# Kernel optimization log

Measured on AMD Instinct MI355X. Metric: run time of the kernel, lower is better.

Reference implementation:

```python
import jax, jax.numpy as jnp
import numpy as np

IN_CH = 256
OUT_CH = 128
N = 6144
ADJ_P = 0.01  # edge density -> avg degree ~61


def setup_inputs() -> dict:
    key = jax.random.key(0)
    ks = jax.random.split(key, 8)
    x = jax.random.normal(ks[0], (1, IN_CH, N), dtype=jnp.float32)
    adj = (jax.random.uniform(ks[1], (N, N)) < ADJ_P).astype(jnp.float32)
    W_fts = jax.random.normal(ks[2], (OUT_CH, IN_CH), dtype=jnp.float32) * 0.05
    w1 = jax.random.normal(ks[3], (OUT_CH,), dtype=jnp.float32) * 0.05
    b1 = jnp.zeros((1,), dtype=jnp.float32)
    w2 = jax.random.normal(ks[4], (OUT_CH,), dtype=jnp.float32) * 0.05
    b2 = jnp.zeros((1,), dtype=jnp.float32)
    vars_bias = jax.random.normal(ks[5], (1, N, OUT_CH), dtype=jnp.float32) * 0.02
    return {"x": x, "adj": adj, "W_fts": W_fts, "w1": w1, "b1": b1,
            "w2": w2, "b2": b2, "vars_bias": vars_bias}


def reference(x, adj, W_fts, w1, b1, w2, b2, vars_bias):
    # fts = Conv1d(in, out, k=1, bias=False)(x): [1, OUT_CH, N]
    fts = jnp.einsum('oi,bin->bon', W_fts, x)
    f = fts[0]  # [OUT_CH, N]
    # f1/f2 = Conv1d(out, 1, 1)(fts) -> per-node scalars [N]
    f1 = jnp.einsum('o,on->n', w1, f) + b1  # [N]
    f2 = jnp.einsum('o,on->n', w2, f) + b2  # [N]
    # scores[i,j] = leaky_relu(adj[i,j]*f1[i] + adj[i,j]*f2[j], 0.2)
    scores = jax.nn.leaky_relu(adj * f1[:, None] + adj * f2[None, :], 0.2)
    # sparse_softmax2d: per-row softmax masked to nonzero entries
    mask = (scores != 0).astype(scores.dtype)
    m = jnp.max(scores, axis=1, keepdims=True)  # stabilizer; cancels in ratio
    exps = jnp.exp(scores - m) * mask
    coefs = exps / jnp.sum(exps, axis=1, keepdims=True)  # [N, N]
    # vals = coefs @ fts.T : [N, OUT_CH]
    vals = coefs @ f.T
    # add bias, permute to [1, OUT_CH, N]
    ret = jnp.transpose(vals[None, :, :] + vars_bias, (0, 2, 1))
    return ret
```

## Files before the change

### kernel.cpp

```cpp
#include <hip/hip_runtime.h>

#define NN  6144
#define ICH 256
#define OCH 128

__global__ __launch_bounds__(256) void k_uproj(const float* __restrict__ W,
        const float* __restrict__ w1, const float* __restrict__ w2,
        float* __restrict__ u1, float* __restrict__ u2) {
    int k = threadIdx.x;
    float a1 = 0.f, a2 = 0.f;
    for (int o = 0; o < OCH; ++o) {
        float wv = W[o * ICH + k];
        a1 = fmaf(w1[o], wv, a1);
        a2 = fmaf(w2[o], wv, a2);
    }
    u1[k] = a1;
    u2[k] = a2;
}

__global__ __launch_bounds__(256) void k_f12(const float* __restrict__ x,
        const float* __restrict__ u1, const float* __restrict__ u2,
        float* __restrict__ f1, float* __restrict__ f2) {
    const int nchunk = blockIdx.x % (NN / 256);
    const int ks     = blockIdx.x / (NN / 256);
    const int n  = nchunk * 256 + threadIdx.x;
    const int k0 = ks * 32;
    float a1 = 0.f, a2 = 0.f;
#pragma unroll
    for (int kk = 0; kk < 32; ++kk) {
        const int k = k0 + kk;
        const float xv = x[(size_t)k * NN + n];
        a1 = fmaf(u1[k], xv, a1);
        a2 = fmaf(u2[k], xv, a2);
    }
    atomicAdd(f1 + n, a1);
    atomicAdd(f2 + n, a2);
}

__global__ __launch_bounds__(256) void k_fts(const float* __restrict__ x,
        const float* __restrict__ W, float* __restrict__ ft) {
    __shared__ float xs[32][32];
    __shared__ float Ws[32][OCH + 4];
    const int n0  = blockIdx.x * 32;
    const int tid = threadIdx.x;
    const int oq = (tid & 31) * 4;
    const int nq = (tid >> 5) * 4;
    float acc[4][4] = {};
    for (int k0 = 0; k0 < ICH; k0 += 32) {
        __syncthreads();
        {
            const int nn = tid & 31;
            const int kb = tid >> 5;
#pragma unroll
            for (int r = 0; r < 4; ++r)
                xs[kb + r * 8][nn] = x[(size_t)(k0 + kb + r * 8) * NN + n0 + nn];
        }
        {
            const int kk = tid & 31;
            const int ob = tid >> 5;
#pragma unroll
            for (int r = 0; r < 16; ++r) {
                const int o = ob + r * 8;
                Ws[kk][o] = W[o * ICH + k0 + kk];
            }
        }
        __syncthreads();
#pragma unroll
        for (int kk = 0; kk < 32; ++kk) {
            const float4 xv = *(const float4*)&xs[kk][nq];
            const float4 wv = *(const float4*)&Ws[kk][oq];
            const float xa[4] = {xv.x, xv.y, xv.z, xv.w};
            const float wa[4] = {wv.x, wv.y, wv.z, wv.w};
#pragma unroll
            for (int a = 0; a < 4; ++a)
#pragma unroll
                for (int b = 0; b < 4; ++b)
                    acc[a][b] = fmaf(xa[a], wa[b], acc[a][b]);
        }
    }
#pragma unroll
    for (int a = 0; a < 4; ++a) {
        float4 v = make_float4(acc[a][0], acc[a][1], acc[a][2], acc[a][3]);
        *(float4*)&ft[(size_t)(n0 + nq + a) * OCH + oq] = v;
    }
}

__global__ __launch_bounds__(256) void k_attn(const float* __restrict__ adj,
        const float* __restrict__ ft, const float* __restrict__ f1,
        const float* __restrict__ f2, const float* __restrict__ b1,
        const float* __restrict__ b2, const float* __restrict__ vb,
        float* __restrict__ out) {
    const int lane = threadIdx.x & 63;
    const int wave = threadIdx.x >> 6;
    const int i = blockIdx.x * 4 + wave;
    const float s1  = f1[i] + b1[0];
    const float bb2 = b2[0];
    const float* arow = adj + (size_t)i * NN;
    float2 nm = make_float2(0.f, 0.f);
    float den = 0.f;
    for (int base = 0; base < NN; base += 256) {
        const int j0 = base + lane * 4;
        const float4 a4 = *(const float4*)(arow + j0);
        float e0 = 0.f, e1 = 0.f, e2 = 0.f, e3 = 0.f;
        const bool any = (a4.x != 0.f) || (a4.y != 0.f) ||
                         (a4.z != 0.f) || (a4.w != 0.f);
        if (any) {
            const float4 g = *(const float4*)(f2 + j0);
            if (a4.x != 0.f) { float s = s1 + g.x + bb2; s = s > 0.f ? s : 0.2f * s; e0 = __expf(s); }
            if (a4.y != 0.f) { float s = s1 + g.y + bb2; s = s > 0.f ? s : 0.2f * s; e1 = __expf(s); }
            if (a4.z != 0.f) { float s = s1 + g.z + bb2; s = s > 0.f ? s : 0.2f * s; e2 = __expf(s); }
            if (a4.w != 0.f) { float s = s1 + g.w + bb2; s = s > 0.f ? s : 0.2f * s; e3 = __expf(s); }
            den += e0 + e1 + e2 + e3;
        }
        unsigned long long m = __ballot(any);
        while (m) {
            const int le = __builtin_ctzll(m);
            m &= m - 1;
            const float v0 = __shfl(e0, le);
            const float v1 = __shfl(e1, le);
            const float v2 = __shfl(e2, le);
            const float v3 = __shfl(e3, le);
            const int jb = base + le * 4;
            if (v0 != 0.f) { const float2 g = *(const float2*)(ft + (size_t)(jb    ) * OCH + 2 * lane);
                             nm.x = fmaf(v0, g.x, nm.x); nm.y = fmaf(v0, g.y, nm.y); }
            if (v1 != 0.f) { const float2 g = *(const float2*)(ft + (size_t)(jb + 1) * OCH + 2 * lane);
                             nm.x = fmaf(v1, g.x, nm.x); nm.y = fmaf(v1, g.y, nm.y); }
            if (v2 != 0.f) { const float2 g = *(const float2*)(ft + (size_t)(jb + 2) * OCH + 2 * lane);
                             nm.x = fmaf(v2, g.x, nm.x); nm.y = fmaf(v2, g.y, nm.y); }
            if (v3 != 0.f) { const float2 g = *(const float2*)(ft + (size_t)(jb + 3) * OCH + 2 * lane);
                             nm.x = fmaf(v3, g.x, nm.x); nm.y = fmaf(v3, g.y, nm.y); }
        }
    }
#pragma unroll
    for (int off = 32; off > 0; off >>= 1) den += __shfl_xor(den, off);
    const float inv = 1.f / den;
    const int c0 = 2 * lane;
    const float2 bv = *(const float2*)(vb + (size_t)i * OCH + c0);
    out[(size_t)(c0    ) * NN + i] = fmaf(nm.x, inv, bv.x);
    out[(size_t)(c0 + 1) * NN + i] = fmaf(nm.y, inv, bv.y);
}

extern "C" void kernel_launch(void* const* d_in, const int* in_sizes, int n_in,
                              void* d_out, int out_size, void* d_ws, size_t ws_size,
                              hipStream_t stream) {
    const float* x   = (const float*)d_in[0];
    const float* adj = (const float*)d_in[1];
    const float* W   = (const float*)d_in[2];
    const float* w1  = (const float*)d_in[3];
    const float* b1  = (const float*)d_in[4];
    const float* w2  = (const float*)d_in[5];
    const float* b2  = (const float*)d_in[6];
    const float* vb  = (const float*)d_in[7];
    float* out = (float*)d_out;

    char* ws = (char*)d_ws;
    float* ft = (float*)ws;
    float* f1 = (float*)(ws + 3145728);
    float* f2 = (float*)(ws + 3145728 + 24576);
    float* u1 = (float*)(ws + 3145728 + 49152);
    float* u2 = u1 + 256;

    hipMemsetAsync(f1, 0, 2 * NN * sizeof(float), stream);
    k_uproj<<<1, 256, 0, stream>>>(W, w1, w2, u1, u2);
    k_f12<<<dim3((NN / 256) * 8), 256, 0, stream>>>(x, u1, u2, f1, f2);
    k_fts<<<dim3(NN / 32), 256, 0, stream>>>(x, W, ft);
    k_attn<<<dim3(NN / 4), 256, 0, stream>>>(adj, ft, f1, f2, b1, b2, vb, out);
}
```

Baseline: 311.4 us.

## Fuse f1/f2 projection into fts GEMM and queue edges per row in attention

Measured after the change: 272.3 us. 1.14x faster.

```diff
diff --git a/kernel.cpp b/kernel.cpp
--- a/kernel.cpp
+++ b/kernel.cpp
@@ -3,42 +3,14 @@
 #define NN  6144
 #define ICH 256
 #define OCH 128
-
-__global__ __launch_bounds__(256) void k_uproj(const float* __restrict__ W,
-        const float* __restrict__ w1, const float* __restrict__ w2,
-        float* __restrict__ u1, float* __restrict__ u2) {
-    int k = threadIdx.x;
-    float a1 = 0.f, a2 = 0.f;
-    for (int o = 0; o < OCH; ++o) {
-        float wv = W[o * ICH + k];
-        a1 = fmaf(w1[o], wv, a1);
-        a2 = fmaf(w2[o], wv, a2);
-    }
-    u1[k] = a1;
-    u2[k] = a2;
-}
-
-__global__ __launch_bounds__(256) void k_f12(const float* __restrict__ x,
-        const float* __restrict__ u1, const float* __restrict__ u2,
-        float* __restrict__ f1, float* __restrict__ f2) {
-    const int nchunk = blockIdx.x % (NN / 256);
-    const int ks     = blockIdx.x / (NN / 256);
-    const int n  = nchunk * 256 + threadIdx.x;
-    const int k0 = ks * 32;
-    float a1 = 0.f, a2 = 0.f;
-#pragma unroll
-    for (int kk = 0; kk < 32; ++kk) {
-        const int k = k0 + kk;
-        const float xv = x[(size_t)k * NN + n];
-        a1 = fmaf(u1[k], xv, a1);
-        a2 = fmaf(u2[k], xv, a2);
-    }
-    atomicAdd(f1 + n, a1);
-    atomicAdd(f2 + n, a2);
-}
+#define WPB 4
+#define NWIN 6
+#define QCAP 256
 
 __global__ __launch_bounds__(256) void k_fts(const float* __restrict__ x,
-        const float* __restrict__ W, float* __restrict__ ft) {
+        const float* __restrict__ W, const float* __restrict__ w1,
+        const float* __restrict__ w2, float* __restrict__ ft,
+        float* __restrict__ f1, float* __restrict__ f2) {
     __shared__ float xs[32][32];
     __shared__ float Ws[32][OCH + 4];
     const int n0  = blockIdx.x * 32;
@@ -83,6 +55,29 @@
         float4 v = make_float4(acc[a][0], acc[a][1], acc[a][2], acc[a][3]);
         *(float4*)&ft[(size_t)(n0 + nq + a) * OCH + oq] = v;
     }
+    const float4 w1v = *(const float4*)(w1 + oq);
+    const float4 w2v = *(const float4*)(w2 + oq);
+    float p1[4], p2[4];
+#pragma unroll
+    for (int a = 0; a < 4; ++a) {
+        p1[a] = acc[a][0] * w1v.x + acc[a][1] * w1v.y + acc[a][2] * w1v.z + acc[a][3] * w1v.w;
+        p2[a] = acc[a][0] * w2v.x + acc[a][1] * w2v.y + acc[a][2] * w2v.z + acc[a][3] * w2v.w;
+    }
+#pragma unroll
+    for (int m = 16; m > 0; m >>= 1) {
+#pragma unroll
+        for (int a = 0; a < 4; ++a) {
+            p1[a] += __shfl_xor(p1[a], m);
+            p2[a] += __shfl_xor(p2[a], m);
+        }
+    }
+    if ((tid & 31) == 0) {
+#pragma unroll
+        for (int a = 0; a < 4; ++a) {
+            f1[n0 + nq + a] = p1[a];
+            f2[n0 + nq + a] = p2[a];
+        }
+    }
 }
 
 __global__ __launch_bounds__(256) void k_attn(const float* __restrict__ adj,
@@ -90,54 +85,68 @@
         const float* __restrict__ f2, const float* __restrict__ b1,
         const float* __restrict__ b2, const float* __restrict__ vb,
         float* __restrict__ out) {
-    const int lane = threadIdx.x & 63;
-    const int wave = threadIdx.x >> 6;
-    const int i = blockIdx.x * 4 + wave;
-    const float s1  = f1[i] + b1[0];
-    const float bb2 = b2[0];
+    __shared__ float q_e[QCAP];
+    __shared__ int   q_j[QCAP];
+    __shared__ int   cnt;
+    __shared__ float dpart[WPB];
+    __shared__ float part[WPB][OCH];
+    const int tid  = threadIdx.x;
+    const int lane = tid & 63;
+    const int wave = tid >> 6;
+    const int i = blockIdx.x;
+    if (tid == 0) cnt = 0;
+    __syncthreads();
+    const float s1 = f1[i] + b1[0] + b2[0];
     const float* arow = adj + (size_t)i * NN;
-    float2 nm = make_float2(0.f, 0.f);
+    const int jbase = wave * (NN / WPB) + lane * 4;
+    float4 a[NWIN];
+#pragma unroll
+    for (int w = 0; w < NWIN; ++w)
+        a[w] = *(const float4*)(arow + jbase + w * 256);
     float den = 0.f;
-    for (int base = 0; base < NN; base += 256) {
-        const int j0 = base + lane * 4;
-        const float4 a4 = *(const float4*)(arow + j0);
-        float e0 = 0.f, e1 = 0.f, e2 = 0.f, e3 = 0.f;
-        const bool any = (a4.x != 0.f) || (a4.y != 0.f) ||
-                         (a4.z != 0.f) || (a4.w != 0.f);
-        if (any) {
+#pragma unroll
+    for (int w = 0; w < NWIN; ++w) {
+        const float4 a4 = a[w];
+        const int j0 = jbase + w * 256;
+        const int k = (a4.x != 0.f) + (a4.y != 0.f) + (a4.z != 0.f) + (a4.w != 0.f);
+        if (k) {
             const float4 g = *(const float4*)(f2 + j0);
-            if (a4.x != 0.f) { float s = s1 + g.x + bb2; s = s > 0.f ? s : 0.2f * s; e0 = __expf(s); }
-            if (a4.y != 0.f) { float s = s1 + g.y + bb2; s = s > 0.f ? s : 0.2f * s; e1 = __expf(s); }
-            if (a4.z != 0.f) { float s = s1 + g.z + bb2; s = s > 0.f ? s : 0.2f * s; e2 = __expf(s); }
-            if (a4.w != 0.f) { float s = s1 + g.w + bb2; s = s > 0.f ? s : 0.2f * s; e3 = __expf(s); }
-            den += e0 + e1 + e2 + e3;
-        }
-        unsigned long long m = __ballot(any);
-        while (m) {
-            const int le = __builtin_ctzll(m);
-            m &= m - 1;
-            const float v0 = __shfl(e0, le);
-            const float v1 = __shfl(e1, le);
-            const float v2 = __shfl(e2, le);
-            const float v3 = __shfl(e3, le);
-            const int jb = base + le * 4;
-            if (v0 != 0.f) { const float2 g = *(const float2*)(ft + (size_t)(jb    ) * OCH + 2 * lane);
-                             nm.x = fmaf(v0, g.x, nm.x); nm.y = fmaf(v0, g.y, nm.y); }
-            if (v1 != 0.f) { const float2 g = *(const float2*)(ft + (size_t)(jb + 1) * OCH + 2 * lane);
-                             nm.x = fmaf(v1, g.x, nm.x); nm.y = fmaf(v1, g.y, nm.y); }
-            if (v2 != 0.f) { const float2 g = *(const float2*)(ft + (size_t)(jb + 2) * OCH + 2 * lane);
-                             nm.x = fmaf(v2, g.x, nm.x); nm.y = fmaf(v2, g.y, nm.y); }
-            if (v3 != 0.f) { const float2 g = *(const float2*)(ft + (size_t)(jb + 3) * OCH + 2 * lane);
-                             nm.x = fmaf(v3, g.x, nm.x); nm.y = fmaf(v3, g.y, nm.y); }
+            int slot = atomicAdd(&cnt, k);
+            if (slot + k <= QCAP) {
+                if (a4.x != 0.f) { float s = s1 + g.x; s = s > 0.f ? s : 0.2f * s;
+                                   float e = __expf(s); den += e; q_j[slot] = j0;     q_e[slot] = e; ++slot; }
+                if (a4.y != 0.f) { float s = s1 + g.y; s = s > 0.f ? s : 0.2f * s;
+                                   float e = __expf(s); den += e; q_j[slot] = j0 + 1; q_e[slot] = e; ++slot; }
+                if (a4.z != 0.f) { float s = s1 + g.z; s = s > 0.f ? s : 0.2f * s;
+                                   float e = __expf(s); den += e; q_j[slot] = j0 + 2; q_e[slot] = e; ++slot; }
+                if (a4.w != 0.f) { float s = s1 + g.w; s = s > 0.f ? s : 0.2f * s;
+                                   float e = __expf(s); den += e; q_j[slot] = j0 + 3; q_e[slot] = e; }
+            }
         }
     }
 #pragma unroll
     for (int off = 32; off > 0; off >>= 1) den += __shfl_xor(den, off);
-    const float inv = 1.f / den;
+    if (lane == 0) dpart[wave] = den;
+    __syncthreads();
+    const int nE = cnt < QCAP ? cnt : QCAP;
+    float2 nm = make_float2(0.f, 0.f);
     const int c0 = 2 * lane;
-    const float2 bv = *(const float2*)(vb + (size_t)i * OCH + c0);
-    out[(size_t)(c0    ) * NN + i] = fmaf(nm.x, inv, bv.x);
-    out[(size_t)(c0 + 1) * NN + i] = fmaf(nm.y, inv, bv.y);
+    for (int idx = wave; idx < nE; idx += WPB) {
+        const int   j = q_j[idx];
+        const float e = q_e[idx];
+        const float2 g = *(const float2*)(ft + (size_t)j * OCH + c0);
+        nm.x = fmaf(e, g.x, nm.x);
+        nm.y = fmaf(e, g.y, nm.y);
+    }
+    part[wave][c0]     = nm.x;
+    part[wave][c0 + 1] = nm.y;
+    __syncthreads();
+    if (tid < OCH) {
+        const float d   = dpart[0] + dpart[1] + dpart[2] + dpart[3];
+        const float inv = 1.f / d;
+        const float v = part[0][tid] + part[1][tid] + part[2][tid] + part[3][tid];
+        out[(size_t)tid * NN + i] = fmaf(v, inv, vb[(size_t)i * OCH + tid]);
+    }
 }
 
 extern "C" void kernel_launch(void* const* d_in, const int* in_sizes, int n_in,
@@ -157,12 +166,7 @@
     float* ft = (float*)ws;
     float* f1 = (float*)(ws + 3145728);
     float* f2 = (float*)(ws + 3145728 + 24576);
-    float* u1 = (float*)(ws + 3145728 + 49152);
-    float* u2 = u1 + 256;
 
-    hipMemsetAsync(f1, 0, 2 * NN * sizeof(float), stream);
-    k_uproj<<<1, 256, 0, stream>>>(W, w1, w2, u1, u2);
-    k_f12<<<dim3((NN / 256) * 8), 256, 0, stream>>>(x, u1, u2, f1, f2);
-    k_fts<<<dim3(NN / 32), 256, 0, stream>>>(x, W, ft);
-    k_attn<<<dim3(NN / 4), 256, 0, stream>>>(adj, ft, f1, f2, b1, b2, vb, out);
+    k_fts<<<dim3(NN / 32), 256, 0, stream>>>(x, W, w1, w2, ft, f1, f2);
+    k_attn<<<dim3(NN), 256, 0, stream>>>(adj, ft, f1, f2, b1, b2, vb, out);
 }
```
